# Performance work log

Hardware: AMD Instinct MI355X
Metric: run time of the kernel (lower is better)

## Reference

```python
import jax, jax.numpy as jnp
import numpy as np

B, S, D, H = 4, 2048, 1024, 16
HEAD = D // H
DENOM = float(np.sqrt(D))  # NOTE: original divides by sqrt(hidden_size), not sqrt(head_size)


def setup_inputs() -> dict:
    key = jax.random.key(0)
    ks = jax.random.split(key, 5)
    scale = 1.0 / np.sqrt(D)
    return {
        "hidden_state": jax.random.normal(ks[0], (B, S, D), dtype=jnp.float32),
        "attention_mask": jnp.ones((B, S), dtype=jnp.int32),  # unused in forward (faithful to source)
        "w_q": jax.random.normal(ks[1], (D, D), dtype=jnp.float32) * scale,
        "w_k": jax.random.normal(ks[2], (D, D), dtype=jnp.float32) * scale,
        "w_v": jax.random.normal(ks[3], (D, D), dtype=jnp.float32) * scale,
        "w_o": jax.random.normal(ks[4], (D, D), dtype=jnp.float32) * scale,
    }


def _split_heads(x):
    # [B, S, D] -> [B, H, S, head]
    b, s, _ = x.shape
    return x.reshape(b, s, H, HEAD).transpose(0, 2, 1, 3)


def reference(hidden_state, attention_mask, w_q, w_k, w_v, w_o):
    # nn.Linear(bias=False): y = x @ W^T with W of shape [out, in]
    q = _split_heads(hidden_state @ w_q.T)  # [B, H, S, head]
    k = _split_heads(hidden_state @ w_k.T)
    v = _split_heads(hidden_state @ w_v.T)
    qk = jnp.einsum("bhqd,bhkd->bhqk", q, k) / DENOM  # scale = 1/sqrt(hidden_size)
    attn = jax.nn.softmax(qk, axis=-1)  # attention_mask is NOT applied (matches source)
    ctx = jnp.einsum("bhqk,bhkd->bhqd", attn, v)  # [B, H, S, head]
    ctx = ctx.transpose(0, 2, 1, 3).reshape(hidden_state.shape[0], hidden_state.shape[1], D)
    return ctx @ w_o.T
```

## Files before the change

kernel.cpp:

```cpp
#include <hip/hip_runtime.h>
#include <hip/hip_bf16.h>
#include <math.h>

typedef __bf16 bf16x8 __attribute__((ext_vector_type(8)));
typedef __bf16 bf16x2 __attribute__((ext_vector_type(2)));
typedef float f32x4 __attribute__((ext_vector_type(4)));
typedef float f32x16 __attribute__((ext_vector_type(16)));
typedef unsigned u32x2v __attribute__((ext_vector_type(2)));
typedef unsigned u32x4v __attribute__((ext_vector_type(4)));
typedef unsigned short u16;

#define QSCALE 0.04508422002778011f

__device__ __forceinline__ u16 f2b(float f) {
  union { float f; unsigned u; } x; x.f = f;
  unsigned r = x.u + 0x7fffu + ((x.u >> 16) & 1u);
  return (u16)(r >> 16);
}

__device__ __forceinline__ unsigned pkbf(float a, float b) {
  bf16x2 t = { (__bf16)a, (__bf16)b };
  return __builtin_bit_cast(unsigned, t);
}

#define GLOAD_LDS16(g, s)                                                      \
  __builtin_amdgcn_global_load_lds(                                            \
      (__attribute__((address_space(1))) void*)(void*)(g),                     \
      (__attribute__((address_space(3))) void*)(s), 16, 0, 0)

__global__ void cast_bf16_kernel(const float* __restrict__ in, u16* __restrict__ out,
                                 int n4) {
  int i = blockIdx.x * blockDim.x + threadIdx.x;
  int stride = gridDim.x * blockDim.x;
  for (; i < n4; i += stride) {
    float4 v = ((const float4*)in)[i];
    ushort4 o;
    o.x = f2b(v.x); o.y = f2b(v.y); o.z = f2b(v.z); o.w = f2b(v.w);
    ((ushort4*)out)[i] = o;
  }
}

__global__ void cast_w4_kernel(const float* __restrict__ wq, const float* __restrict__ wk,
                               const float* __restrict__ wv, const float* __restrict__ wo,
                               u16* __restrict__ wqkv, u16* __restrict__ wob) {
  const int w = blockIdx.y;
  const float* src = (w == 0) ? wq : (w == 1) ? wk : (w == 2) ? wv : wo;
  u16* dst = (w < 3) ? wqkv + (size_t)w * 1024 * 1024 : wob;
  const float scale = (w == 0) ? QSCALE : 1.0f;
  const int n4 = 1024 * 1024 / 4;
  int i = blockIdx.x * blockDim.x + threadIdx.x;
  int stride = gridDim.x * blockDim.x;
  for (; i < n4; i += stride) {
    float4 v = ((const float4*)src)[i];
    ushort4 o;
    o.x = f2b(v.x * scale); o.y = f2b(v.y * scale);
    o.z = f2b(v.z * scale); o.w = f2b(v.w * scale);
    ((ushort4*)dst)[i] = o;
  }
}

template <int OUT_MODE>
__global__ __launch_bounds__(256) void gemm_nt64(const u16* __restrict__ A,
                                                 const u16* __restrict__ B,
                                                 void* __restrict__ O0,
                                                 u16* __restrict__ Ko,
                                                 u16* __restrict__ Vt) {
  __shared__ u16 As[128 * 64];
  __shared__ u16 Bs[128 * 64];
  const int tid = threadIdx.x;
  const int wid = tid >> 6, lane = tid & 63;
  const int fr = lane & 15, fg = lane >> 4;
  const int wr = wid >> 1, wc = wid & 1;
  const int m0 = blockIdx.y * 128, n0 = blockIdx.x * 128;
  const int K = 1024;

  f32x4 acc[4][4] = {};

  for (int kt = 0; kt < K; kt += 64) {
#pragma unroll
    for (int i2 = 0; i2 < 4; ++i2) {
      int c = i2 * 256 + tid;
      int row = c >> 3, sl = c & 7;
      int kc = sl ^ (row & 7);
      GLOAD_LDS16(A + (size_t)(m0 + row) * K + kt + kc * 8, (char*)As + c * 16);
      GLOAD_LDS16(B + (size_t)(n0 + row) * K + kt + kc * 8, (char*)Bs + c * 16);
    }
    __syncthreads();

    bf16x8 af[4][2], bfr[4][2];
#pragma unroll
    for (int m = 0; m < 4; ++m) {
      const int row = wr * 64 + m * 16 + fr;
#pragma unroll
      for (int ks = 0; ks < 2; ++ks)
        af[m][ks] = *(const bf16x8*)((const char*)As + row * 128 +
                                     ((ks * 64 + fg * 16) ^ ((fr & 7) << 4)));
    }
#pragma unroll
    for (int n = 0; n < 4; ++n) {
      const int row = wc * 64 + n * 16 + fr;
#pragma unroll
      for (int ks = 0; ks < 2; ++ks)
        bfr[n][ks] = *(const bf16x8*)((const char*)Bs + row * 128 +
                                      ((ks * 64 + fg * 16) ^ ((fr & 7) << 4)));
    }
    __builtin_amdgcn_s_setprio(1);
#pragma unroll
    for (int m = 0; m < 4; ++m)
#pragma unroll
      for (int n = 0; n < 4; ++n)
#pragma unroll
        for (int ks = 0; ks < 2; ++ks)
          acc[m][n] = __builtin_amdgcn_mfma_f32_16x16x32_bf16(af[m][ks], bfr[n][ks],
                                                              acc[m][n], 0, 0, 0);
    __builtin_amdgcn_s_setprio(0);
    __syncthreads();
  }

#pragma unroll
  for (int m = 0; m < 4; ++m)
#pragma unroll
    for (int n = 0; n < 4; ++n) {
      int gr = m0 + wr * 64 + m * 16 + fg * 4;
      int gc = n0 + wc * 64 + n * 16 + fr;
      if (OUT_MODE == 0) {
#pragma unroll
        for (int j = 0; j < 4; ++j)
          ((float*)O0)[(size_t)(gr + j) * 1024 + gc] = acc[m][n][j];
      } else {
        const int region = n0 >> 10;
        if (region == 2) {
          int vc = gc - 2048;
          int hh = vc >> 6, dd = vc & 63, bb2 = gr >> 11, s0 = gr & 2047;
          ushort4 o;
          o.x = f2b(acc[m][n][0]); o.y = f2b(acc[m][n][1]);
          o.z = f2b(acc[m][n][2]); o.w = f2b(acc[m][n][3]);
          *(ushort4*)(Vt + (((size_t)bb2 * 16 + hh) * 64 + dd) * 2048 + s0) = o;
        } else {
          u16* dst = (region == 0) ? (u16*)O0 : Ko;
          int cc = gc & 1023;
#pragma unroll
          for (int j = 0; j < 4; ++j)
            dst[(size_t)(gr + j) * 1024 + cc] = f2b(acc[m][n][j]);
        }
      }
    }
}

__global__ __launch_bounds__(256, 2) void attn_fwd(const u16* __restrict__ Q,
                                                   const u16* __restrict__ Kg,
                                                   const u16* __restrict__ Vtg,
                                                   u16* __restrict__ O) {
  __shared__ u16 Ks[2][64 * 64];
  __shared__ u16 Vs[2][64 * 64];
  const int tid = threadIdx.x;
  const int wid = tid >> 6, lane = tid & 63;
  const int lq = lane & 31, hi = lane >> 5;
  const int id = blockIdx.x;
  const int swz = (id & 7) * 64 + (id >> 3);
  const int qb = swz & 7, bh = swz >> 3;
  const int b = bh >> 4, h = bh & 15;
  const size_t tokBase = (size_t)b * 2048 * 1024 + h * 64;
  const size_t vBase = (size_t)bh * 64 * 2048;
  const int q0 = qb * 256 + wid * 64;

  bf16x8 qfA[4], qfB[4];
#pragma unroll
  for (int s = 0; s < 4; ++s) {
    qfA[s] = *(const bf16x8*)(Q + tokBase + (size_t)(q0 + lq) * 1024 + s * 16 + hi * 8);
    qfB[s] = *(const bf16x8*)(Q + tokBase + (size_t)(q0 + 32 + lq) * 1024 + s * 16 + hi * 8);
  }

  f32x16 accA0 = {}, accA1 = {}, accB0 = {}, accB1 = {};
  f32x16 lsvA = {}, lsvB = {};

  const int skey = tid >> 3, sdc = tid & 7;
  const int sdg = sdc ^ (skey & 7);
  const int skey2 = (tid + 256) >> 3;
  const int sdg2 = sdc ^ (skey2 & 7);

#define STAGE(bb_, k0_) do {                                                          \
    GLOAD_LDS16(Kg + tokBase + (size_t)((k0_) + skey) * 1024 + sdg * 8,               \
                (char*)Ks[bb_] + tid * 16);                                           \
    GLOAD_LDS16(Kg + tokBase + (size_t)((k0_) + skey2) * 1024 + sdg2 * 8,             \
                (char*)Ks[bb_] + (tid + 256) * 16);                                   \
    GLOAD_LDS16(Vtg + vBase + (size_t)skey * 2048 + (k0_) + sdg * 8,                  \
                (char*)Vs[bb_] + tid * 16);                                           \
    GLOAD_LDS16(Vtg + vBase + (size_t)skey2 * 2048 + (k0_) + sdg2 * 8,                \
                (char*)Vs[bb_] + (tid + 256) * 16);                                   \
  } while (0)

  STAGE(0, 0);
  for (int t = 0; t < 32; ++t) {
    const int bb = t & 1;
    __syncthreads();
    if (t < 31) STAGE(bb ^ 1, (t + 1) * 64);

    f32x16 svA0 = {}, svA1 = {}, svB0 = {}, svB1 = {};
    __builtin_amdgcn_s_setprio(1);
#pragma unroll
    for (int s = 0; s < 4; ++s) {
      bf16x8 kf0 = *(const bf16x8*)((const char*)Ks[bb] + lq * 128 +
                                    ((s * 32 + hi * 16) ^ ((lq & 7) << 4)));
      bf16x8 kf1 = *(const bf16x8*)((const char*)Ks[bb] + (32 + lq) * 128 +
                                    ((s * 32 + hi * 16) ^ ((lq & 7) << 4)));
      svA0 = __builtin_amdgcn_mfma_f32_32x32x16_bf16(kf0, qfA[s], svA0, 0, 0, 0);
      svB0 = __builtin_amdgcn_mfma_f32_32x32x16_bf16(kf0, qfB[s], svB0, 0, 0, 0);
      svA1 = __builtin_amdgcn_mfma_f32_32x32x16_bf16(kf1, qfA[s], svA1, 0, 0, 0);
      svB1 = __builtin_amdgcn_mfma_f32_32x32x16_bf16(kf1, qfB[s], svB1, 0, 0, 0);
    }
    __builtin_amdgcn_s_setprio(0);

#pragma unroll
    for (int i = 0; i < 16; ++i) svA0[i] = __builtin_amdgcn_exp2f(svA0[i]);
#pragma unroll
    for (int i = 0; i < 16; ++i) svA1[i] = __builtin_amdgcn_exp2f(svA1[i]);
#pragma unroll
    for (int i = 0; i < 16; ++i) svB0[i] = __builtin_amdgcn_exp2f(svB0[i]);
#pragma unroll
    for (int i = 0; i < 16; ++i) svB1[i] = __builtin_amdgcn_exp2f(svB1[i]);
    lsvA += svA0; lsvA += svA1;
    lsvB += svB0; lsvB += svB1;

    bf16x8 paA[4], paB[4];
#pragma unroll
    for (int kb = 0; kb < 2; ++kb) {
#pragma unroll
      for (int hh = 0; hh < 2; ++hh) {
        const int rb = hh * 8;
        {
          const f32x16& pv = kb ? svA1 : svA0;
          unsigned w01 = pkbf(pv[rb + 0], pv[rb + 1]);
          unsigned w23 = pkbf(pv[rb + 2], pv[rb + 3]);
          unsigned w45 = pkbf(pv[rb + 4], pv[rb + 5]);
          unsigned w67 = pkbf(pv[rb + 6], pv[rb + 7]);
          u32x2v ra = __builtin_amdgcn_permlane32_swap(w01, w45, false, false);
          u32x2v rc = __builtin_amdgcn_permlane32_swap(w23, w67, false, false);
          u32x4v fw = { ra[0], rc[0], ra[1], rc[1] };
          paA[kb * 2 + hh] = __builtin_bit_cast(bf16x8, fw);
        }
        {
          const f32x16& pv = kb ? svB1 : svB0;
          unsigned w01 = pkbf(pv[rb + 0], pv[rb + 1]);
          unsigned w23 = pkbf(pv[rb + 2], pv[rb + 3]);
          unsigned w45 = pkbf(pv[rb + 4], pv[rb + 5]);
          unsigned w67 = pkbf(pv[rb + 6], pv[rb + 7]);
          u32x2v ra = __builtin_amdgcn_permlane32_swap(w01, w45, false, false);
          u32x2v rc = __builtin_amdgcn_permlane32_swap(w23, w67, false, false);
          u32x4v fw = { ra[0], rc[0], ra[1], rc[1] };
          paB[kb * 2 + hh] = __builtin_bit_cast(bf16x8, fw);
        }
      }
    }

    __builtin_amdgcn_s_setprio(1);
#pragma unroll
    for (int s = 0; s < 4; ++s) {
      bf16x8 bv0 = *(const bf16x8*)((const char*)Vs[bb] + lq * 128 +
                                    ((s * 32 + hi * 16) ^ ((lq & 7) << 4)));
      bf16x8 bv1 = *(const bf16x8*)((const char*)Vs[bb] + (32 + lq) * 128 +
                                    ((s * 32 + hi * 16) ^ ((lq & 7) << 4)));
      accA0 = __builtin_amdgcn_mfma_f32_32x32x16_bf16(paA[s], bv0, accA0, 0, 0, 0);
      accA1 = __builtin_amdgcn_mfma_f32_32x32x16_bf16(paA[s], bv1, accA1, 0, 0, 0);
      accB0 = __builtin_amdgcn_mfma_f32_32x32x16_bf16(paB[s], bv0, accB0, 0, 0, 0);
      accB1 = __builtin_amdgcn_mfma_f32_32x32x16_bf16(paB[s], bv1, accB1, 0, 0, 0);
    }
    __builtin_amdgcn_s_setprio(0);
  }
#undef STAGE

  float totA = 0.f, totB = 0.f;
#pragma unroll
  for (int i = 0; i < 16; ++i) { totA += lsvA[i]; totB += lsvB[i]; }
  totA += __shfl_xor(totA, 32);
  totB += __shfl_xor(totB, 32);
  const float invA = 1.0f / totA, invB = 1.0f / totB;
#pragma unroll
  for (int r = 0; r < 16; ++r) {
    const int q = (r & 3) + 8 * (r >> 2) + 4 * hi;
    const float ivA = __shfl(invA, q);
    const float ivB = __shfl(invB, q);
    const size_t rowA = (size_t)(b * 2048 + q0 + q) * 1024 + h * 64;
    const size_t rowB = (size_t)(b * 2048 + q0 + 32 + q) * 1024 + h * 64;
    O[rowA + lq]      = f2b(accA0[r] * ivA);
    O[rowA + 32 + lq] = f2b(accA1[r] * ivA);
    O[rowB + lq]      = f2b(accB0[r] * ivB);
    O[rowB + 32 + lq] = f2b(accB1[r] * ivB);
  }
}

extern "C" void kernel_launch(void* const* d_in, const int* in_sizes, int n_in,
                              void* d_out, int out_size, void* d_ws, size_t ws_size,
                              hipStream_t stream) {
  const float* hs = (const float*)d_in[0];
  const float* wq = (const float*)d_in[2];
  const float* wk = (const float*)d_in[3];
  const float* wv = (const float*)d_in[4];
  const float* wo = (const float*)d_in[5];

  const size_t TOK = 8192, DD = 1024;
  u16* hsb  = (u16*)d_ws;
  u16* wqkv = hsb + TOK * DD;
  u16* wob  = wqkv + 3 * DD * DD;
  u16* Qb   = wob + DD * DD;
  u16* Kb   = Qb + TOK * DD;
  u16* Vtg  = Kb + TOK * DD;
  u16* Cb   = Vtg + TOK * DD;

  cast_bf16_kernel<<<2048, 256, 0, stream>>>(hs, hsb, (int)(TOK * DD / 4));
  cast_w4_kernel<<<dim3(128, 4), 256, 0, stream>>>(wq, wk, wv, wo, wqkv, wob);

  gemm_nt64<1><<<dim3(24, 64), 256, 0, stream>>>(hsb, wqkv, Qb, Kb, Vtg);

  attn_fwd<<<dim3(512), 256, 0, stream>>>(Qb, Kb, Vtg, Cb);

  gemm_nt64<0><<<dim3(8, 64), 256, 0, stream>>>(Cb, wob, d_out, nullptr, nullptr);
}
```

Measured before the change: 190.6 us.

## Merge cast kernels, XCD-swizzle GEMM blocks, load V directly to registers

Merges the activation and weight cast kernels into one launch, removing one kernel launch. Remaps the GEMM grid to 1D with an XCD-aware swizzle so neighbouring tiles share L2 on the same die. In attention, V fragments are now read straight from global memory into registers instead of being staged through double-buffered LDS, which halves LDS use and LDS traffic. The cost is exposed global-load latency for V inside the loop. The cast grid of 512x5 blocks also leaves the large hidden-state cast to only 512 blocks.

```diff
diff --git a/kernel.cpp b/kernel.cpp
--- a/kernel.cpp
+++ b/kernel.cpp
@@ -28,26 +28,18 @@
       (__attribute__((address_space(1))) void*)(void*)(g),                     \
       (__attribute__((address_space(3))) void*)(s), 16, 0, 0)
 
-__global__ void cast_bf16_kernel(const float* __restrict__ in, u16* __restrict__ out,
-                                 int n4) {
-  int i = blockIdx.x * blockDim.x + threadIdx.x;
-  int stride = gridDim.x * blockDim.x;
-  for (; i < n4; i += stride) {
-    float4 v = ((const float4*)in)[i];
-    ushort4 o;
-    o.x = f2b(v.x); o.y = f2b(v.y); o.z = f2b(v.z); o.w = f2b(v.w);
-    ((ushort4*)out)[i] = o;
-  }
-}
-
-__global__ void cast_w4_kernel(const float* __restrict__ wq, const float* __restrict__ wk,
-                               const float* __restrict__ wv, const float* __restrict__ wo,
-                               u16* __restrict__ wqkv, u16* __restrict__ wob) {
+__global__ void cast_all_kernel(const float* __restrict__ hs,
+                                const float* __restrict__ wq, const float* __restrict__ wk,
+                                const float* __restrict__ wv, const float* __restrict__ wo,
+                                u16* __restrict__ hsb, u16* __restrict__ wqkv,
+                                u16* __restrict__ wob) {
   const int w = blockIdx.y;
-  const float* src = (w == 0) ? wq : (w == 1) ? wk : (w == 2) ? wv : wo;
-  u16* dst = (w < 3) ? wqkv + (size_t)w * 1024 * 1024 : wob;
-  const float scale = (w == 0) ? QSCALE : 1.0f;
-  const int n4 = 1024 * 1024 / 4;
+  const float* src; u16* dst; int n4; float scale = 1.0f;
+  if (w == 0)      { src = hs; dst = hsb;                 n4 = 8192 * 1024 / 4; }
+  else if (w == 1) { src = wq; dst = wqkv;                n4 = 1024 * 1024 / 4; scale = QSCALE; }
+  else if (w == 2) { src = wk; dst = wqkv + 1024 * 1024;  n4 = 1024 * 1024 / 4; }
+  else if (w == 3) { src = wv; dst = wqkv + 2 * 1024 * 1024; n4 = 1024 * 1024 / 4; }
+  else             { src = wo; dst = wob;                 n4 = 1024 * 1024 / 4; }
   int i = blockIdx.x * blockDim.x + threadIdx.x;
   int stride = gridDim.x * blockDim.x;
   for (; i < n4; i += stride) {
@@ -64,14 +56,19 @@
                                                  const u16* __restrict__ B,
                                                  void* __restrict__ O0,
                                                  u16* __restrict__ Ko,
-                                                 u16* __restrict__ Vt) {
+                                                 u16* __restrict__ Vt,
+                                                 int nbx) {
   __shared__ u16 As[128 * 64];
   __shared__ u16 Bs[128 * 64];
   const int tid = threadIdx.x;
   const int wid = tid >> 6, lane = tid & 63;
   const int fr = lane & 15, fg = lane >> 4;
   const int wr = wid >> 1, wc = wid & 1;
-  const int m0 = blockIdx.y * 128, n0 = blockIdx.x * 128;
+  const int id = blockIdx.x;
+  const int cpx = gridDim.x >> 3;
+  const int swzid = (id & 7) * cpx + (id >> 3);
+  const int by = swzid / nbx, bx = swzid % nbx;
+  const int m0 = by * 128, n0 = bx * 128;
   const int K = 1024;
 
   f32x4 acc[4][4] = {};
@@ -152,7 +149,6 @@
                                                    const u16* __restrict__ Vtg,
                                                    u16* __restrict__ O) {
   __shared__ u16 Ks[2][64 * 64];
-  __shared__ u16 Vs[2][64 * 64];
   const int tid = threadIdx.x;
   const int wid = tid >> 6, lane = tid & 63;
   const int lq = lane & 31, hi = lane >> 5;
@@ -171,6 +167,9 @@
     qfB[s] = *(const bf16x8*)(Q + tokBase + (size_t)(q0 + 32 + lq) * 1024 + s * 16 + hi * 8);
   }
 
+  const u16* Vp0 = Vtg + vBase + (size_t)lq * 2048 + hi * 8;
+  const u16* Vp1 = Vtg + vBase + (size_t)(32 + lq) * 2048 + hi * 8;
+
   f32x16 accA0 = {}, accA1 = {}, accB0 = {}, accB1 = {};
   f32x16 lsvA = {}, lsvB = {};
 
@@ -179,22 +178,27 @@
   const int skey2 = (tid + 256) >> 3;
   const int sdg2 = sdc ^ (skey2 & 7);
 
-#define STAGE(bb_, k0_) do {                                                          \
+#define STAGE_K(bb_, k0_) do {                                                        \
     GLOAD_LDS16(Kg + tokBase + (size_t)((k0_) + skey) * 1024 + sdg * 8,               \
                 (char*)Ks[bb_] + tid * 16);                                           \
     GLOAD_LDS16(Kg + tokBase + (size_t)((k0_) + skey2) * 1024 + sdg2 * 8,             \
                 (char*)Ks[bb_] + (tid + 256) * 16);                                   \
-    GLOAD_LDS16(Vtg + vBase + (size_t)skey * 2048 + (k0_) + sdg * 8,                  \
-                (char*)Vs[bb_] + tid * 16);                                           \
-    GLOAD_LDS16(Vtg + vBase + (size_t)skey2 * 2048 + (k0_) + sdg2 * 8,                \
-                (char*)Vs[bb_] + (tid + 256) * 16);                                   \
   } while (0)
 
-  STAGE(0, 0);
+  STAGE_K(0, 0);
   for (int t = 0; t < 32; ++t) {
     const int bb = t & 1;
+    const int k0 = t * 64;
     __syncthreads();
-    if (t < 31) STAGE(bb ^ 1, (t + 1) * 64);
+
+    bf16x8 bv0[4], bv1[4];
+#pragma unroll
+    for (int s = 0; s < 4; ++s) {
+      bv0[s] = *(const bf16x8*)(Vp0 + k0 + s * 16);
+      bv1[s] = *(const bf16x8*)(Vp1 + k0 + s * 16);
+    }
+
+    if (t < 31) STAGE_K(bb ^ 1, (t + 1) * 64);
 
     f32x16 svA0 = {}, svA1 = {}, svB0 = {}, svB1 = {};
     __builtin_amdgcn_s_setprio(1);
@@ -256,18 +260,14 @@
     __builtin_amdgcn_s_setprio(1);
 #pragma unroll
     for (int s = 0; s < 4; ++s) {
-      bf16x8 bv0 = *(const bf16x8*)((const char*)Vs[bb] + lq * 128 +
-                                    ((s * 32 + hi * 16) ^ ((lq & 7) << 4)));
-      bf16x8 bv1 = *(const bf16x8*)((const char*)Vs[bb] + (32 + lq) * 128 +
-                                    ((s * 32 + hi * 16) ^ ((lq & 7) << 4)));
-      accA0 = __builtin_amdgcn_mfma_f32_32x32x16_bf16(paA[s], bv0, accA0, 0, 0, 0);
-      accA1 = __builtin_amdgcn_mfma_f32_32x32x16_bf16(paA[s], bv1, accA1, 0, 0, 0);
-      accB0 = __builtin_amdgcn_mfma_f32_32x32x16_bf16(paB[s], bv0, accB0, 0, 0, 0);
-      accB1 = __builtin_amdgcn_mfma_f32_32x32x16_bf16(paB[s], bv1, accB1, 0, 0, 0);
+      accA0 = __builtin_amdgcn_mfma_f32_32x32x16_bf16(paA[s], bv0[s], accA0, 0, 0, 0);
+      accA1 = __builtin_amdgcn_mfma_f32_32x32x16_bf16(paA[s], bv1[s], accA1, 0, 0, 0);
+      accB0 = __builtin_amdgcn_mfma_f32_32x32x16_bf16(paB[s], bv0[s], accB0, 0, 0, 0);
+      accB1 = __builtin_amdgcn_mfma_f32_32x32x16_bf16(paB[s], bv1[s], accB1, 0, 0, 0);
     }
     __builtin_amdgcn_s_setprio(0);
   }
-#undef STAGE
+#undef STAGE_K
 
   float totA = 0.f, totB = 0.f;
 #pragma unroll
@@ -307,12 +307,11 @@
   u16* Vtg  = Kb + TOK * DD;
   u16* Cb   = Vtg + TOK * DD;
 
-  cast_bf16_kernel<<<2048, 256, 0, stream>>>(hs, hsb, (int)(TOK * DD / 4));
-  cast_w4_kernel<<<dim3(128, 4), 256, 0, stream>>>(wq, wk, wv, wo, wqkv, wob);
-
-  gemm_nt64<1><<<dim3(24, 64), 256, 0, stream>>>(hsb, wqkv, Qb, Kb, Vtg);
+  cast_all_kernel<<<dim3(512, 5), 256, 0, stream>>>(hs, wq, wk, wv, wo, hsb, wqkv, wob);
+
+  gemm_nt64<1><<<1536, 256, 0, stream>>>(hsb, wqkv, Qb, Kb, Vtg, 24);
 
   attn_fwd<<<dim3(512), 256, 0, stream>>>(Qb, Kb, Vtg, Cb);
 
-  gemm_nt64<0><<<dim3(8, 64), 256, 0, stream>>>(Cb, wob, d_out, nullptr, nullptr);
-}
+  gemm_nt64<0><<<512, 256, 0, stream>>>(Cb, wob, d_out, nullptr, nullptr, 8);
+}
```

After: 237.8 us. 24.7% more time.
